# Kernel optimization log

Hardware: AMD Instinct MI355X
Metric: run time of the kernel (lower is better)

Reference implementation:

```python
import jax, jax.numpy as jnp
import numpy as np

# Model dims (match init_kwargs)
B, T, DIM = 2, 2048, 1024
SEG = 8                 # num_segments
SD = DIM // SEG         # 128, per-segment feature dim
E = 16                  # num_routed_experts
K = 2                   # top-k routing (assumed; not in init signature)
H_SH = 4 * DIM          # shared expert hidden
H_R = 4 * SD            # routed expert hidden


def setup_inputs() -> dict:
    key = jax.random.key(0)
    ks = jax.random.split(key, 10)
    s = 0.02
    return {
        "X": jax.random.normal(ks[0], (B, T, DIM), jnp.float32),
        # shared expert (num_shared_experts = 1): FFN dim -> 4*dim -> dim
        "Ws1": jax.random.normal(ks[1], (DIM, H_SH), jnp.float32) * s,
        "bs1": jnp.zeros((H_SH,), jnp.float32),
        "Ws2": jax.random.normal(ks[2], (H_SH, DIM), jnp.float32) * s,
        "bs2": jnp.zeros((DIM,), jnp.float32),
        # router over segment features
        "Wr": jax.random.normal(ks[3], (SD, E), jnp.float32) * s,
        # routed expert array: per-expert FFN sd -> 4*sd -> sd
        "We1": jax.random.normal(ks[4], (E, SD, H_R), jnp.float32) * s,
        "be1": jnp.zeros((E, H_R), jnp.float32),
        "We2": jax.random.normal(ks[5], (E, H_R, SD), jnp.float32) * s,
        "be2": jnp.zeros((E, SD), jnp.float32),
    }


def reference(X, Ws1, bs1, Ws2, bs2, Wr, We1, be1, We2, be2):
    Bb, Tt, C = X.shape
    # segments: [B, S, T, sd]
    xs = X.reshape(Bb, Tt, SEG, SD).transpose(0, 2, 1, 3)

    # shared expert(s) on full-width tokens
    shared = jax.nn.gelu(X @ Ws1 + bs1) @ Ws2 + bs2  # [B,T,C]

    # router: softmax over experts then top-k per token-segment
    probs = jax.nn.softmax(xs @ Wr, axis=-1)            # [B,S,T,E]
    w, idx = jax.lax.top_k(probs, K)                    # [B,S,T,K]
    onehot = jax.nn.one_hot(idx, E, dtype=X.dtype)      # [B,S,T,K,E]
    # per-token combine weight for each expert (top-k distinct => at most one)
    w_e = jnp.einsum('bstke,bstk->bste', onehot, w)     # [B,S,T,E]

    # weighted expert compute + scatter-add, expressed as masked dense combine
    routed = jnp.zeros_like(xs)
    for e in range(E):  # fixed small expert loop
        h = jax.nn.gelu(xs @ We1[e] + be1[e])           # [B,S,T,H_R]
        y = h @ We2[e] + be2[e]                         # [B,S,T,sd]
        routed = routed + w_e[..., e:e + 1] * y

    # switch-style aux load-balance loss (assumed compute_aux_loss)
    f = onehot.sum(3).reshape(-1, E).mean(0) / K        # dispatch fraction
    P = w_e.reshape(-1, E).mean(0)                      # mean combine weight
    aux_loss = E * jnp.sum(f * P)

    out = shared + routed.transpose(0, 2, 1, 3).reshape(Bb, Tt, C)
    return out, aux_loss
```

## Files before the change

### kernel.cpp

```cpp
#include <hip/hip_runtime.h>
#include <stdint.h>

#define DIMC 1024
#define TOK  4096
#define SEGN 8
#define SD   128
#define NE   16
#define RSEG 32768
#define HSH  4096
#define HR   512

#define BM 128
#define BN 128
#define BK 32

#define MAXT   528
#define MAXPAD (MAXT * BM)

using bf16x8 = __attribute__((ext_vector_type(8))) __bf16;
using f32x4  = __attribute__((ext_vector_type(4))) float;

__device__ __forceinline__ unsigned short f2bf(float f) {
  unsigned int x = __builtin_bit_cast(unsigned int, f);
  unsigned int r = (x + 0x7fffu + ((x >> 16) & 1u)) >> 16;
  return (unsigned short)r;
}

__device__ __forceinline__ float gelu_f(float x) {
  float u2 = -1.5957691216057308f * (x + 0.044715f * x * x * x);
  return x / (1.f + __expf(u2));
}

#define GLDS(gp, lp) __builtin_amdgcn_global_load_lds( \
    (const __attribute__((address_space(1))) void*)(gp), \
    (__attribute__((address_space(3))) void*)(lp), 16, 0, 0)

template <int EPI, bool SWZ, bool SPARSE>
__global__ __launch_bounds__(256) void gemm_bt(
    const unsigned short* __restrict__ A,
    const unsigned short* __restrict__ BT,
    const float* __restrict__ bias,
    float* __restrict__ Cf,
    unsigned short* __restrict__ Cb,
    int N, int K,
    const int* __restrict__ tileE, const int* __restrict__ tileR,
    const int* __restrict__ perm, const float* __restrict__ wgt,
    long btStride, int biasStride)
{
  __shared__ unsigned short As[BM * BK];
  __shared__ unsigned short Bs[BN * BK];
  const int t = threadIdx.x;
  const int w = t >> 6, l = t & 63;

  int bx = blockIdx.x, by = blockIdx.y;
  if (SWZ) {
    int gx = gridDim.x;
    int nwg = gx * gridDim.y;
    int flat = by * gx + bx;
    int q = nwg >> 3, r0 = nwg & 7;
    int xcd = flat & 7, j = flat >> 3;
    flat = (xcd < r0 ? xcd * (q + 1) : r0 * (q + 1) + (xcd - r0) * q) + j;
    bx = flat % gx; by = flat / gx;
  }

  long mBase;
  if (SPARSE) {
    int te = tileE[by];
    if (te < 0) return;
    mBase = tileR[by];
    BT += (long)te * btStride;
    bias += (long)te * biasStride;
  } else {
    mBase = (long)by * BM;
  }
  const long nBase = (long)bx * BN;
  const int wm = w >> 1, wn = w & 1;

  const int rowc = w * 16 + (l >> 2);
  const int colE = (l & 3) * 8;
  const unsigned short *gA0, *gA1;
  if (SPARSE && EPI == 0) {
    int r0 = perm[mBase + rowc];
    int r1 = perm[mBase + 64 + rowc];
    gA0 = A + (long)(r0 < 0 ? 0 : r0) * K + colE;
    gA1 = A + (long)(r1 < 0 ? 0 : r1) * K + colE;
  } else {
    gA0 = A + (mBase + rowc) * (long)K + colE;
    gA1 = A + (mBase + 64 + rowc) * (long)K + colE;
  }
  const unsigned short* gB0 = BT + (nBase + rowc) * (long)K + colE;
  const unsigned short* gB1 = BT + (nBase + 64 + rowc) * (long)K + colE;
  unsigned short* lA0 = &As[(w * 16) * BK];
  unsigned short* lA1 = &As[(64 + w * 16) * BK];
  unsigned short* lB0 = &Bs[(w * 16) * BK];
  unsigned short* lB1 = &Bs[(64 + w * 16) * BK];

  f32x4 acc[4][4] = {};

  const int ar = l & 15;
  const int ak = (l >> 4) * 8;

  for (int kt = 0; kt < K; kt += BK) {
    GLDS(gA0 + kt, lA0);
    GLDS(gA1 + kt, lA1);
    GLDS(gB0 + kt, lB0);
    GLDS(gB1 + kt, lB1);
    __syncthreads();
    bf16x8 av[4], bv[4];
#pragma unroll
    for (int f = 0; f < 4; ++f)
      av[f] = *(const bf16x8*)&As[(wm * 64 + f * 16 + ar) * BK + ak];
#pragma unroll
    for (int g = 0; g < 4; ++g)
      bv[g] = *(const bf16x8*)&Bs[(wn * 64 + g * 16 + ar) * BK + ak];
#pragma unroll
    for (int f = 0; f < 4; ++f)
#pragma unroll
      for (int g = 0; g < 4; ++g)
        acc[f][g] = __builtin_amdgcn_mfma_f32_16x16x32_bf16(av[f], bv[g], acc[f][g], 0, 0, 0);
    __syncthreads();
  }

  const int cr = (l >> 4) * 4;
  const int cc = l & 15;
#pragma unroll
  for (int f = 0; f < 4; ++f) {
#pragma unroll
    for (int j = 0; j < 4; ++j) {
      long gr = mBase + wm * 64 + f * 16 + cr + j;
      int ri = 0;
      float wv = 0.f;
      if (EPI == 3) {
        ri = perm[gr];
        wv = (ri >= 0) ? wgt[gr] : 0.f;
      }
#pragma unroll
      for (int g = 0; g < 4; ++g) {
        long gc = nBase + wn * 64 + g * 16 + cc;
        float v = acc[f][g][j] + bias[gc];
        if (EPI == 0) {
          Cb[gr * N + gc] = f2bf(gelu_f(v));
        } else if (EPI == 1) {
          Cf[gr * N + gc] = v;
        } else {
          if (ri >= 0) atomicAdd(&Cf[(long)ri * N + gc], wv * v);
        }
      }
    }
  }
}

__global__ void conv_x(const float* __restrict__ X, unsigned short* __restrict__ Xb) {
  int i = blockIdx.x * 256 + threadIdx.x;
  float4 v = reinterpret_cast<const float4*>(X)[i];
  union { unsigned short h[4]; uint2 u; } r;
  r.h[0] = f2bf(v.x); r.h[1] = f2bf(v.y); r.h[2] = f2bf(v.z); r.h[3] = f2bf(v.w);
  reinterpret_cast<uint2*>(Xb)[i] = r.u;
}

__global__ void transpose_conv(const float* __restrict__ in, unsigned short* __restrict__ out,
                               int K, int N, long long inStride, long long outStride) {
  __shared__ float tile[32][33];
  const float* ip = in + (long long)blockIdx.z * inStride;
  unsigned short* op = out + (long long)blockIdx.z * outStride;
  int k0 = blockIdx.y * 32, n0 = blockIdx.x * 32;
  int tx = threadIdx.x, ty = threadIdx.y;
#pragma unroll
  for (int j = 0; j < 32; j += 8)
    tile[ty + j][tx] = ip[(long long)(k0 + ty + j) * N + n0 + tx];
  __syncthreads();
#pragma unroll
  for (int j = 0; j < 32; j += 8)
    op[(long long)(n0 + ty + j) * K + k0 + tx] = f2bf(tile[tx][ty + j]);
}

__global__ void router_kernel(const float* __restrict__ X, const float* __restrict__ Wr,
                              int* __restrict__ idx0, int* __restrict__ idx1,
                              float* __restrict__ w0, float* __restrict__ w1,
                              unsigned int* __restrict__ cntI,
                              float* __restrict__ wsum) {
  __shared__ unsigned int s_cnt[NE];
  __shared__ float s_wsum[NE];
  int t = threadIdx.x;
  if (t < NE) { s_cnt[t] = 0u; s_wsum[t] = 0.f; }
  __syncthreads();
  int r = blockIdx.x * 256 + t;
  const float* x = X + (long)r * SD;
  float logit[NE];
#pragma unroll
  for (int e = 0; e < NE; e++) logit[e] = 0.f;
  for (int k = 0; k < SD; k++) {
    float xv = x[k];
    const float* wr = Wr + k * NE;
#pragma unroll
    for (int e = 0; e < NE; e++) logit[e] += xv * wr[e];
  }
  float m = logit[0];
#pragma unroll
  for (int e = 1; e < NE; e++) m = fmaxf(m, logit[e]);
  int i0 = 0; float q0 = logit[0];
#pragma unroll
  for (int e = 1; e < NE; e++) if (logit[e] > q0) { q0 = logit[e]; i0 = e; }
  int i1 = -1; float q1 = -3.4e38f;
#pragma unroll
  for (int e = 0; e < NE; e++) if (e != i0 && logit[e] > q1) { q1 = logit[e]; i1 = e; }
  float s = 0.f;
#pragma unroll
  for (int e = 0; e < NE; e++) s += __expf(logit[e] - m);
  float inv = 1.f / s;
  float W0 = __expf(q0 - m) * inv, W1 = __expf(q1 - m) * inv;
  idx0[r] = i0; idx1[r] = i1; w0[r] = W0; w1[r] = W1;
  atomicAdd(&s_cnt[i0], 1u); atomicAdd(&s_cnt[i1], 1u);
  atomicAdd(&s_wsum[i0], W0); atomicAdd(&s_wsum[i1], W1);
  __syncthreads();
  if (t < NE) { atomicAdd(&cntI[t], s_cnt[t]); atomicAdd(&wsum[t], s_wsum[t]); }
}

__global__ void build_tiles(const unsigned int* __restrict__ cntI,
                            int* __restrict__ off, int* __restrict__ tileE,
                            int* __restrict__ tileR) {
  int o = 0, t = 0;
  for (int e = 0; e < NE; e++) {
    off[e] = o;
    int c = (int)cntI[e];
    int nt = (c + BM - 1) / BM;
    for (int k = 0; k < nt; k++) { tileE[t] = e; tileR[t] = o + k * BM; t++; }
    o += nt * BM;
  }
  for (; t < MAXT; t++) { tileE[t] = -1; tileR[t] = 0; }
}

__global__ void scatter_perm(const int* __restrict__ idx0, const int* __restrict__ idx1,
                             const float* __restrict__ w0, const float* __restrict__ w1,
                             const int* __restrict__ off, unsigned int* __restrict__ fill,
                             int* __restrict__ perm, float* __restrict__ wgt) {
  __shared__ unsigned int s_cnt[NE];
  __shared__ unsigned int s_base[NE];
  int t = threadIdx.x;
  if (t < NE) s_cnt[t] = 0u;
  __syncthreads();
  int r = blockIdx.x * 256 + t;
  int e0 = idx0[r], e1 = idx1[r];
  unsigned int rk0 = atomicAdd(&s_cnt[e0], 1u);
  unsigned int rk1 = atomicAdd(&s_cnt[e1], 1u);
  __syncthreads();
  if (t < NE) s_base[t] = atomicAdd(&fill[t], s_cnt[t]);
  __syncthreads();
  int loc0 = off[e0] + (int)(s_base[e0] + rk0);
  perm[loc0] = r; wgt[loc0] = w0[r];
  int loc1 = off[e1] + (int)(s_base[e1] + rk1);
  perm[loc1] = r; wgt[loc1] = w1[r];
}

__global__ void aux_finalize(const unsigned int* __restrict__ cntI,
                             const float* __restrict__ wsum, float* __restrict__ outAux) {
  float srt = 0.f;
  for (int e = 0; e < NE; e++) {
    float f = (float)cntI[e] / (float)(RSEG * 2);
    float P = wsum[e] / (float)RSEG;
    srt += f * P;
  }
  *outAux = (float)NE * srt;
}

extern "C" void kernel_launch(void* const* d_in, const int* in_sizes, int n_in,
                              void* d_out, int out_size, void* d_ws, size_t ws_size,
                              hipStream_t stream) {
  (void)in_sizes; (void)n_in; (void)out_size; (void)ws_size;
  const float* X   = (const float*)d_in[0];
  const float* Ws1 = (const float*)d_in[1];
  const float* bs1 = (const float*)d_in[2];
  const float* Ws2 = (const float*)d_in[3];
  const float* bs2 = (const float*)d_in[4];
  const float* Wr  = (const float*)d_in[5];
  const float* We1 = (const float*)d_in[6];
  const float* be1 = (const float*)d_in[7];
  const float* We2 = (const float*)d_in[8];
  const float* be2 = (const float*)d_in[9];
  float* out = (float*)d_out;

  char* p = (char*)d_ws;
  auto alloc = [&](size_t bytes) -> char* {
    char* q = p; p += (bytes + 511) & ~(size_t)511; return q;
  };
  unsigned short* Xb = (unsigned short*)alloc((size_t)TOK * DIMC * 2);
  char* region1 = alloc((size_t)MAXPAD * HR * 2);
  unsigned short* Hg   = (unsigned short*)region1;
  unsigned short* Ws1T = (unsigned short*)region1;
  unsigned short* Ws2T = (unsigned short*)(region1 + (size_t)HSH * DIMC * 2);
  unsigned short* H1b  = (unsigned short*)(region1 + (size_t)2 * HSH * DIMC * 2);
  unsigned short* We1T = (unsigned short*)alloc((size_t)NE * HR * SD * 2);
  unsigned short* We2T = (unsigned short*)alloc((size_t)NE * SD * HR * 2);
  int*   idx0p = (int*)alloc((size_t)RSEG * 4);
  int*   idx1p = (int*)alloc((size_t)RSEG * 4);
  float* w0p   = (float*)alloc((size_t)RSEG * 4);
  float* w1p   = (float*)alloc((size_t)RSEG * 4);
  int*   permp = (int*)alloc((size_t)MAXPAD * 4);
  float* wgtp  = (float*)alloc((size_t)MAXPAD * 4);
  unsigned int* cntI = (unsigned int*)alloc(NE * 4);
  unsigned int* fill = (unsigned int*)alloc(NE * 4);
  int*   offp  = (int*)alloc(NE * 4);
  int*   tileE = (int*)alloc(MAXT * 4);
  int*   tileR = (int*)alloc(MAXT * 4);
  float* wsum  = (float*)alloc(NE * 4);

  hipMemsetAsync(cntI, 0, NE * 4, stream);
  hipMemsetAsync(fill, 0, NE * 4, stream);
  hipMemsetAsync(wsum, 0, NE * 4, stream);
  hipMemsetAsync(permp, 0xFF, (size_t)MAXPAD * 4, stream);

  conv_x<<<TOK * DIMC / 4 / 256, 256, 0, stream>>>(X, Xb);
  dim3 tb(32, 8);
  transpose_conv<<<dim3(HSH / 32, DIMC / 32, 1), tb, 0, stream>>>(Ws1, Ws1T, DIMC, HSH, 0, 0);
  transpose_conv<<<dim3(DIMC / 32, HSH / 32, 1), tb, 0, stream>>>(Ws2, Ws2T, HSH, DIMC, 0, 0);
  transpose_conv<<<dim3(HR / 32, SD / 32, NE), tb, 0, stream>>>(We1, We1T, SD, HR, (long long)SD * HR, (long long)HR * SD);
  transpose_conv<<<dim3(SD / 32, HR / 32, NE), tb, 0, stream>>>(We2, We2T, HR, SD, (long long)HR * SD, (long long)SD * HR);

  router_kernel<<<RSEG / 256, 256, 0, stream>>>(X, Wr, idx0p, idx1p, w0p, w1p, cntI, wsum);
  build_tiles<<<1, 1, 0, stream>>>(cntI, offp, tileE, tileR);
  scatter_perm<<<RSEG / 256, 256, 0, stream>>>(idx0p, idx1p, w0p, w1p, offp, fill, permp, wgtp);
  aux_finalize<<<1, 1, 0, stream>>>(cntI, wsum, out + (size_t)TOK * DIMC);

  gemm_bt<0, true, false><<<dim3(HSH / BN, TOK / BM), 256, 0, stream>>>(
      Xb, Ws1T, bs1, nullptr, H1b, HSH, DIMC, nullptr, nullptr, nullptr, nullptr, 0, 0);
  gemm_bt<1, true, false><<<dim3(DIMC / BN, TOK / BM), 256, 0, stream>>>(
      H1b, Ws2T, bs2, out, nullptr, DIMC, HSH, nullptr, nullptr, nullptr, nullptr, 0, 0);

  gemm_bt<0, false, true><<<dim3(HR / BN, MAXT), 256, 0, stream>>>(
      Xb, We1T, be1, nullptr, Hg, HR, SD, tileE, tileR, permp, wgtp, (long)HR * SD, HR);
  gemm_bt<3, false, true><<<dim3(SD / BN, MAXT), 256, 0, stream>>>(
      Hg, We2T, be2, out, nullptr, SD, HR, tileE, tileR, permp, wgtp, (long)SD * HR, SD);
}
```

Baseline: 408.0 us.

## Split-K the shared down-projection GEMM and parallelize tile building

The second shared-expert GEMM (K=4096, only 8x32=256 tiles) is split four ways along K over blockIdx.z. Partial sums are accumulated into a pre-zeroed output with float atomics, and the bias is added only by the first split. This is meant to raise occupancy on a GPU with many CUs, at the cost of an extra memset of the output and atomic write traffic. Separately, build_tiles now fills its tile tables with 256 threads instead of a single thread.

```diff
diff --git a/kernel.cpp b/kernel.cpp
--- a/kernel.cpp
+++ b/kernel.cpp
@@ -35,7 +35,7 @@
     (const __attribute__((address_space(1))) void*)(gp), \
     (__attribute__((address_space(3))) void*)(lp), 16, 0, 0)
 
-template <int EPI, bool SWZ, bool SPARSE>
+template <int EPI, bool SWZ, bool SPARSE, int SPLITK>
 __global__ __launch_bounds__(256) void gemm_bt(
     const unsigned short* __restrict__ A,
     const unsigned short* __restrict__ BT,
@@ -62,6 +62,8 @@
     flat = (xcd < r0 ? xcd * (q + 1) : r0 * (q + 1) + (xcd - r0) * q) + j;
     bx = flat % gx; by = flat / gx;
   }
+  const int kz = (SPLITK > 1) ? blockIdx.z : 0;
+  const int Ks = K / SPLITK;
 
   long mBase;
   if (SPARSE) {
@@ -100,7 +102,7 @@
   const int ar = l & 15;
   const int ak = (l >> 4) * 8;
 
-  for (int kt = 0; kt < K; kt += BK) {
+  for (int kt = kz * Ks; kt < (kz + 1) * Ks; kt += BK) {
     GLDS(gA0 + kt, lA0);
     GLDS(gA1 + kt, lA1);
     GLDS(gB0 + kt, lB0);
@@ -137,11 +139,12 @@
 #pragma unroll
       for (int g = 0; g < 4; ++g) {
         long gc = nBase + wn * 64 + g * 16 + cc;
-        float v = acc[f][g][j] + bias[gc];
+        float bb = (kz == 0) ? bias[gc] : 0.f;
+        float v = acc[f][g][j] + bb;
         if (EPI == 0) {
           Cb[gr * N + gc] = f2bf(gelu_f(v));
-        } else if (EPI == 1) {
-          Cf[gr * N + gc] = v;
+        } else if (EPI == 4) {
+          atomicAdd(&Cf[gr * N + gc], v);
         } else {
           if (ri >= 0) atomicAdd(&Cf[(long)ri * N + gc], wv * v);
         }
@@ -219,15 +222,29 @@
 __global__ void build_tiles(const unsigned int* __restrict__ cntI,
                             int* __restrict__ off, int* __restrict__ tileE,
                             int* __restrict__ tileR) {
-  int o = 0, t = 0;
-  for (int e = 0; e < NE; e++) {
-    off[e] = o;
-    int c = (int)cntI[e];
-    int nt = (c + BM - 1) / BM;
-    for (int k = 0; k < nt; k++) { tileE[t] = e; tileR[t] = o + k * BM; t++; }
-    o += nt * BM;
-  }
-  for (; t < MAXT; t++) { tileE[t] = -1; tileR[t] = 0; }
+  __shared__ int ts[NE + 1];
+  __shared__ int bs[NE];
+  int t = threadIdx.x;
+  if (t == 0) {
+    int o = 0, tt = 0;
+    for (int e = 0; e < NE; e++) {
+      off[e] = o; ts[e] = tt; bs[e] = o;
+      int nt = ((int)cntI[e] + BM - 1) / BM;
+      tt += nt; o += nt * BM;
+    }
+    ts[NE] = tt;
+  }
+  __syncthreads();
+  int total = ts[NE];
+  for (int i = t; i < MAXT; i += 256) {
+    if (i >= total) { tileE[i] = -1; tileR[i] = 0; }
+    else {
+      int e = 0;
+#pragma unroll
+      for (int k = 1; k < NE; k++) if (ts[k] <= i) e = k;
+      tileE[i] = e; tileR[i] = bs[e] + (i - ts[e]) * BM;
+    }
+  }
 }
 
 __global__ void scatter_perm(const int* __restrict__ idx0, const int* __restrict__ idx1,
@@ -308,6 +325,7 @@
   hipMemsetAsync(fill, 0, NE * 4, stream);
   hipMemsetAsync(wsum, 0, NE * 4, stream);
   hipMemsetAsync(permp, 0xFF, (size_t)MAXPAD * 4, stream);
+  hipMemsetAsync(out, 0, (size_t)TOK * DIMC * 4, stream);
 
   conv_x<<<TOK * DIMC / 4 / 256, 256, 0, stream>>>(X, Xb);
   dim3 tb(32, 8);
@@ -317,17 +335,17 @@
   transpose_conv<<<dim3(SD / 32, HR / 32, NE), tb, 0, stream>>>(We2, We2T, HR, SD, (long long)HR * SD, (long long)SD * HR);
 
   router_kernel<<<RSEG / 256, 256, 0, stream>>>(X, Wr, idx0p, idx1p, w0p, w1p, cntI, wsum);
-  build_tiles<<<1, 1, 0, stream>>>(cntI, offp, tileE, tileR);
+  build_tiles<<<1, 256, 0, stream>>>(cntI, offp, tileE, tileR);
   scatter_perm<<<RSEG / 256, 256, 0, stream>>>(idx0p, idx1p, w0p, w1p, offp, fill, permp, wgtp);
   aux_finalize<<<1, 1, 0, stream>>>(cntI, wsum, out + (size_t)TOK * DIMC);
 
-  gemm_bt<0, true, false><<<dim3(HSH / BN, TOK / BM), 256, 0, stream>>>(
+  gemm_bt<0, true, false, 1><<<dim3(HSH / BN, TOK / BM), 256, 0, stream>>>(
       Xb, Ws1T, bs1, nullptr, H1b, HSH, DIMC, nullptr, nullptr, nullptr, nullptr, 0, 0);
-  gemm_bt<1, true, false><<<dim3(DIMC / BN, TOK / BM), 256, 0, stream>>>(
+  gemm_bt<4, true, false, 4><<<dim3(DIMC / BN, TOK / BM, 4), 256, 0, stream>>>(
       H1b, Ws2T, bs2, out, nullptr, DIMC, HSH, nullptr, nullptr, nullptr, nullptr, 0, 0);
 
-  gemm_bt<0, false, true><<<dim3(HR / BN, MAXT), 256, 0, stream>>>(
+  gemm_bt<0, false, true, 1><<<dim3(HR / BN, MAXT), 256, 0, stream>>>(
       Xb, We1T, be1, nullptr, Hg, HR, SD, tileE, tileR, permp, wgtp, (long)HR * SD, HR);
-  gemm_bt<3, false, true><<<dim3(SD / BN, MAXT), 256, 0, stream>>>(
+  gemm_bt<3, false, true, 1><<<dim3(SD / BN, MAXT), 256, 0, stream>>>(
       Hg, We2T, be2, out, nullptr, SD, HR, tileE, tileR, permp, wgtp, (long)SD * HR, SD);
 }
```

New measurement: 411.6 us. About the same (+0.9%).
